# Kernel optimization log

Hardware: AMD Instinct MI355X
Metric: run time of the kernel (lower is better)

The kernel has to match this reference:

```python
import jax, jax.numpy as jnp
import numpy as np
import math

D_MODEL = 512
HEADS = 8
SHIFT = 1
B, T = 2, 1024


def _layernorm(x, w, b, eps=1e-5):
    mu = jnp.mean(x, -1, keepdims=True)
    var = jnp.mean((x - mu) ** 2, -1, keepdims=True)
    return (x - mu) / jnp.sqrt(var + eps) * w + b


def _l1_cdist(x, w, chunk):
    # x: [N, Din], w: [M, Din] -> [N, M]; chunk over M to bound the broadcast buffer
    N, Din = x.shape
    M = w.shape[0]
    wc = w.reshape(M // chunk, chunk, Din)
    f = lambda wb: jnp.abs(x[:, None, :] - wb[None, :, :]).sum(-1)  # [N, chunk]
    out = jax.lax.map(f, wc)  # [M//chunk, N, chunk]
    return jnp.moveaxis(out, 0, 1).reshape(N, M)


def _proxy_linear(x, w, gain, chunk):
    # ProxyDeltaLinearV68: out = (0.5 - dist_proxy_mean) * gain, dist uses detach trick
    Bx, Tx, Din = x.shape
    xa = jnp.tanh(x).reshape(-1, Din)
    wa = jnp.tanh(w)
    l1 = _l1_cdist(xa, wa, chunk)
    # squared L2 via GEMM (== cdist(p=2)**2), clamped at 0 like torch.cdist
    l2 = jnp.maximum((xa * xa).sum(-1)[:, None] + (wa * wa).sum(-1)[None, :] - 2.0 * (xa @ wa.T), 0.0)
    l1m = l1 / Din
    l2m = l2 / Din
    d = jax.lax.stop_gradient(l1m - l2m) + l2m
    return ((0.5 - d) * gain[None, :]).reshape(Bx, Tx, -1)


def _attention(x, wq_w, wq_g, wk_w, wk_g, wv_w, wv_g, wo_w, wo_b, gamma, rho):
    Bx, Tx, C = x.shape
    H, Dh = HEADS, C // HEADS

    def heads(t):
        return t.reshape(Bx, Tx, H, Dh).transpose(0, 2, 1, 3).reshape(Bx * H, Tx, Dh)

    q = heads(jnp.tanh(_proxy_linear(x, wq_w, wq_g, 32)))
    k = heads(jnp.tanh(_proxy_linear(x, wk_w, wk_g, 32)))
    v = heads(_proxy_linear(x, wv_w, wv_g, 32))
    # pairwise L1 distances, chunked over query positions
    TC = 64
    qr = jnp.moveaxis(q.reshape(Bx * H, Tx // TC, TC, Dh), 1, 0)  # [Tx//TC, BH, TC, Dh]
    f = lambda qb: jnp.abs(qb[:, :, None, :] - k[:, None, :, :]).sum(-1)  # [BH, TC, Tx]
    l1 = jnp.moveaxis(jax.lax.map(f, qr), 0, 1).reshape(Bx * H, Tx, Tx)
    l2 = jnp.maximum((q * q).sum(-1)[:, :, None] + (k * k).sum(-1)[:, None, :]
                     - 2.0 * jnp.einsum('btd,bsd->bts', q, k), 0.0)
    dist = jax.lax.stop_gradient((l1 - l2) / Dh) + l2 / Dh
    dist = dist.reshape(Bx, H, Tx, Tx) * math.sqrt(Dh)
    dsq = dist * dist
    gp = jax.nn.softplus(gamma)[None, :, None, None]
    rp = jax.nn.softplus(rho)[None, :, None, None]
    aw = (1.0 / (1.0 + gp * dsq + 1e-6)) ** rp  # student-t style kernel
    mask = jnp.tril(jnp.ones((Tx, Tx), dtype=bool))
    aw = jnp.where(mask[None, None], aw, 0.0)
    probs = aw / (aw.sum(-1, keepdims=True) + 1e-6)
    out = jnp.einsum('bhts,bhsd->bhtd', probs, v.reshape(Bx, H, Tx, Dh))
    out = out.transpose(0, 2, 1, 3).reshape(Bx, Tx, C)
    return out @ wo_w.T + wo_b


def setup_inputs() -> dict:
    key = jax.random.key(0)
    ks = jax.random.split(key, 10)
    D, Hd = D_MODEL, D_MODEL * 4
    f32 = jnp.float32
    return {
        'x': jax.random.normal(ks[0], (B, T, D), f32),
        'ln1_w': jnp.ones((D,), f32), 'ln1_b': jnp.zeros((D,), f32),
        'wq_w': jax.random.normal(ks[1], (D, D), f32) * 0.1, 'wq_g': jnp.full((D,), 2.0, f32),
        'wk_w': jax.random.normal(ks[2], (D, D), f32) * 0.1, 'wk_g': jnp.full((D,), 2.0, f32),
        'wv_w': jax.random.normal(ks[3], (D, D), f32) * 0.1, 'wv_g': jnp.full((D,), 2.0, f32),
        'wo_w': jax.random.normal(ks[4], (D, D), f32) * 0.02, 'wo_b': jnp.zeros((D,), f32),
        'gamma': jnp.ones((HEADS,), f32), 'rho': jnp.full((HEADS,), 2.0, f32),
        'ln2_w': jnp.ones((D,), f32), 'ln2_b': jnp.zeros((D,), f32),
        'gate_w': jax.random.normal(ks[5], (Hd, D), f32) * 0.1, 'gate_g': jnp.full((Hd,), 2.0, f32),
        'val_w': jax.random.normal(ks[6], (Hd, D), f32) * 0.1, 'val_g': jnp.full((Hd,), 2.0, f32),
        'out_w': jax.random.normal(ks[7], (D, Hd), f32) * 0.1, 'out_g': jnp.full((D,), 2.0, f32),
        'dir_w': jax.random.normal(ks[8], (D,), f32) * 0.1,
    }


def reference(x, ln1_w, ln1_b, wq_w, wq_g, wk_w, wk_g, wv_w, wv_g, wo_w, wo_b,
              gamma, rho, ln2_w, ln2_b, gate_w, gate_g, val_w, val_g, out_w, out_g, dir_w):
    a = _attention(_layernorm(x, ln1_w, ln1_b), wq_w, wq_g, wk_w, wk_g, wv_w, wv_g,
                   wo_w, wo_b, gamma, rho)
    x = x + a  # ATTN_SCALE = 1.0
    h = _layernorm(x, ln2_w, ln2_b)
    gate = jax.nn.silu(_proxy_linear(h, gate_w, gate_g, 32))
    val = _proxy_linear(h, val_w, val_g, 32)
    f = _proxy_linear(gate * val, out_w, out_g, 8)
    # Direction: causal shift of ln2 output, |x_shift - sigmoid(w)|
    xp = jnp.concatenate([jnp.zeros((x.shape[0], SHIFT, x.shape[2]), x.dtype), h[:, :-SHIFT]], axis=1)
    d = jnp.abs(xp - jax.nn.sigmoid(dir_w)[None, None, :])
    return x + f + 0.5 * d  # Delta_SCALE=1.0, DIR_SCALE=0.5, dropout identity (eval)
```

## Files before the change

### kernel.cpp

```cpp
#include <hip/hip_runtime.h>
#include <math.h>


#define NROWS  2048
#define DMODEL 512
#define TSEQ   1024
#define HIDDEN 2048

typedef _Float16 hf;
typedef hf h2 __attribute__((ext_vector_type(2)));
typedef hf h4 __attribute__((ext_vector_type(4)));
typedef hf h8 __attribute__((ext_vector_type(8)));
typedef float f32x4 __attribute__((ext_vector_type(4)));

#if defined(__has_builtin)
#if __has_builtin(__builtin_amdgcn_sad_u8)
#define HAVE_SAD 1
#endif
#if __has_builtin(__builtin_amdgcn_mfma_f32_16x16x32_f16)
#define HAVE_MFMA 1
#endif
#endif

__device__ __forceinline__ unsigned sad8(unsigned a, unsigned b, unsigned c) {
#ifdef HAVE_SAD
  return __builtin_amdgcn_sad_u8(a, b, c);
#else
  unsigned r;
  asm("v_sad_u8 %0, %1, %2, %3" : "=v"(r) : "v"(a), "v"(b), "v"(c));
  return r;
#endif
}

__device__ __forceinline__ float ftanh(float x) {
  const float t = __expf(-2.0f * fabsf(x));
  const float r = (1.0f - t) / (1.0f + t);
  return copysignf(r, x);
}

__device__ __forceinline__ float fpow_ge1(float x, float p) {
  float lg, r;
  asm("v_log_f32 %0, %1" : "=v"(lg) : "v"(x));
  const float e = lg * p;
  asm("v_exp_f32 %0, %1" : "=v"(r) : "v"(e));
  return r;
}

__device__ __forceinline__ unsigned q8(float x) {
  return (unsigned)(int)((x + 1.0f) * 127.5f + 0.5f);
}

struct CP { const float* g0; const float* g1; const float* g2; };

__global__ __launch_bounds__(256) void ln_kernel(
    const float* __restrict__ X, const float* __restrict__ w,
    const float* __restrict__ bb, float* __restrict__ outPlain,
    unsigned char* __restrict__ out8)
{
  const int n = blockIdx.x, tid = threadIdx.x;
  const float* row = X + (size_t)n * DMODEL;
  float2 v = *(const float2*)&row[tid * 2];
  float s1 = v.x + v.y;
  float s2 = v.x * v.x + v.y * v.y;
#pragma unroll
  for (int off = 1; off < 64; off <<= 1) {
    s1 += __shfl_xor(s1, off);
    s2 += __shfl_xor(s2, off);
  }
  __shared__ float red[8];
  if ((tid & 63) == 0) { red[(tid >> 6) * 2] = s1; red[(tid >> 6) * 2 + 1] = s2; }
  __syncthreads();
  s1 = red[0] + red[2] + red[4] + red[6];
  s2 = red[1] + red[3] + red[5] + red[7];
  const float mu   = s1 * (1.0f / DMODEL);
  const float var  = s2 * (1.0f / DMODEL) - mu * mu;
  const float rstd = rsqrtf(var + 1e-5f);
  const int d = tid * 2;
  const float y0 = (v.x - mu) * rstd * w[d]     + bb[d];
  const float y1 = (v.y - mu) * rstd * w[d + 1] + bb[d + 1];
  if (outPlain) *(float2*)&outPlain[(size_t)n * DMODEL + d] = make_float2(y0, y1);
  const unsigned a = q8(ftanh(y0)), b = q8(ftanh(y1));
  *(unsigned short*)&out8[(size_t)n * DMODEL + d] = (unsigned short)(a | (b << 8));
}

__global__ __launch_bounds__(256) void tanhcvt8m_kernel(
    const float* __restrict__ s0, const float* __restrict__ s1,
    const float* __restrict__ s2, unsigned char* __restrict__ out, int K)
{
  const int z = blockIdx.y;
  const float* sb = (z == 0) ? s0 : (z == 1) ? s1 : s2;
  const int rows = (int)gridDim.x * 2;
  const int row = blockIdx.x * 2 + (threadIdx.x >> 7);
  const int t = threadIdx.x & 127;
  const float* src = sb + (size_t)row * K;
  unsigned char* dst = out + ((size_t)z * rows + row) * K;
  for (int k = t * 4; k < K; k += 512) {
    float4 v = *(const float4*)&src[k];
    unsigned pk = q8(ftanh(v.x)) | (q8(ftanh(v.y)) << 8) |
                  (q8(ftanh(v.z)) << 16) | (q8(ftanh(v.w)) << 24);
    *(unsigned*)&dst[k] = pk;
  }
}

template <int NCD, int EPI>
__global__ __launch_bounds__(256, 8) void cdistn_kernel(
    const unsigned char* __restrict__ X8, const unsigned char* __restrict__ W8,
    CP cp,
    unsigned char* __restrict__ o8a, unsigned char* __restrict__ o8b,
    hf* __restrict__ vt16, unsigned char* __restrict__ gvt8,
    unsigned short* __restrict__ pf,
    int M, int K, int Kc, float invK127)
{
  const int m0 = blockIdx.x * 32, n0 = blockIdx.y * 64;
  const int zc = (EPI == 1) ? blockIdx.z : 0;
  const int kb = (EPI == 3) ? blockIdx.z * Kc : 0;
  __shared__ unsigned xs8[2][8][68];
  __shared__ unsigned ws8[2][8][NCD * 36];
  const int tid = threadIdx.x, tx = tid & 15, ty = tid >> 4;
  unsigned acc[NCD][4][2] = {};

  const int rs = tid >> 2, pxs = (tid & 3) * 2;
  const int half = tid & 127;
  const int wc = (NCD == 2) ? (tid >> 7) : 0;
  const int wcol = half >> 2, pws = (half & 3) * 2;

  const unsigned char* xp = X8 + (size_t)(n0 + rs) * K + kb + (tid & 3) * 8;
  const unsigned char* wq = W8 + (size_t)(zc + wc) * M * K +
                            (size_t)(m0 + wcol) * K + kb + (half & 3) * 8;

  uint2 xv = *(const uint2*)xp;
  uint2 wv = *(const uint2*)wq;

  int p = 0;
#pragma unroll 1
  for (int k0 = 0; k0 < Kc; k0 += 32) {
    xs8[p][pxs + 0][rs] = xv.x;
    xs8[p][pxs + 1][rs] = xv.y;
    ws8[p][pws + 0][wc * 36 + wcol] = wv.x;
    ws8[p][pws + 1][wc * 36 + wcol] = wv.y;
    const int kn = (k0 + 32 < Kc) ? k0 + 32 : 0;
    xv = *(const uint2*)(xp + kn);
    wv = *(const uint2*)(wq + kn);
    __syncthreads();

#pragma unroll
    for (int kk = 0; kk < 8; kk++) {
      uint4 a4 = *(const uint4*)&xs8[p][kk][ty * 4];
      const unsigned a[4] = {a4.x, a4.y, a4.z, a4.w};
#pragma unroll
      for (int c = 0; c < NCD; c++) {
        uint2 b2 = *(const uint2*)&ws8[p][kk][c * 36 + tx * 2];
        const unsigned bb[2] = {b2.x, b2.y};
#pragma unroll
        for (int i = 0; i < 4; i++)
#pragma unroll
          for (int j = 0; j < 2; j++)
            acc[c][i][j] = sad8(a[i], bb[j], acc[c][i][j]);
      }
    }
    p ^= 1;
  }

  if constexpr (EPI == 1) {
    if (zc < 2) {
      unsigned char* o8 = zc ? o8b : o8a;
      const float* gn = zc ? cp.g1 : cp.g0;
#pragma unroll
      for (int i = 0; i < 4; i++) {
        const int n = n0 + ty * 4 + i;
        unsigned pk = 0;
#pragma unroll
        for (int j = 0; j < 2; j++) {
          const int m = m0 + tx * 2 + j;
          const float val = (0.5f - (float)acc[0][i][j] * invK127) * gn[m];
          pk |= q8(ftanh(val)) << (8 * j);
        }
        *(unsigned short*)&o8[(size_t)n * M + m0 + tx * 2] = (unsigned short)pk;
      }
    } else {
#pragma unroll
      for (int i = 0; i < 4; i++) {
        const int n = n0 + ty * 4 + i;
        const int b = n >> 10, t = n & 1023;
#pragma unroll
        for (int j = 0; j < 2; j++) {
          const int m = m0 + tx * 2 + j;
          const float vv = (0.5f - (float)acc[0][i][j] * invK127) * cp.g2[m];
          vt16[((size_t)(b * 8 + (m >> 6)) * 64 + (m & 63)) * 1024 + t] = (hf)vv;
        }
      }
    }
  } else if constexpr (EPI == 2) {
#pragma unroll
    for (int i = 0; i < 4; i++) {
      const int n = n0 + ty * 4 + i;
      unsigned pk = 0;
#pragma unroll
      for (int j = 0; j < 2; j++) {
        const int m = m0 + tx * 2 + j;
        float g = (0.5f - (float)acc[0][i][j] * invK127) * cp.g0[m];
        g = g / (1.0f + __expf(-g));
        const float vv = (0.5f - (float)acc[1][i][j] * invK127) * cp.g1[m];
        pk |= q8(ftanh(g * vv)) << (8 * j);
      }
      *(unsigned short*)&gvt8[(size_t)n * M + m0 + tx * 2] = (unsigned short)pk;
    }
  } else {
    unsigned short* pz = pf + (size_t)blockIdx.z * ((size_t)NROWS * M);
#pragma unroll
    for (int i = 0; i < 4; i++) {
      const int n = n0 + ty * 4 + i;
      const unsigned p0 = (acc[0][i][0] + 1) >> 1;
      const unsigned p1 = (acc[0][i][1] + 1) >> 1;
      *(unsigned*)&pz[(size_t)n * M + m0 + tx * 2] = p0 | (p1 << 16);
    }
  }
}

__global__ __launch_bounds__(256) void attn_part_kernel(
    const unsigned char* __restrict__ Qb, const unsigned char* __restrict__ Kb,
    const hf* __restrict__ Vt,
    const float* __restrict__ gamma, const float* __restrict__ rho,
    float* __restrict__ accO, float* __restrict__ accR)
{
  const int bh = blockIdx.y, b = bh >> 3, h = bh & 7;
  int rem = 143 - (int)blockIdx.x;
  int tt = 0;
  for (;;) {
    const int nc = ((tt >> 1) + 2) >> 1;
    if (rem < nc) break;
    rem -= nc; ++tt;
  }
  const int ntile = (tt >> 1) + 1;
  const int sb = rem * 2;
  const int se = (sb + 2 < ntile) ? sb + 2 : ntile;
  const int t0 = tt * 32;

  const float gp = log1pf(expf(gamma[h]));
  const float nrp = -log1pf(expf(rho[h]));
  const size_t base8 = ((size_t)b * TSEQ) * DMODEL + h * 64;

  __shared__ unsigned qs8[16][36];
  __shared__ unsigned ks8[16][68];
  __shared__ hf awt[32][72];
  __shared__ hf vsm[64][72];

  const int tid = threadIdx.x, tx = tid & 15, ty = tid >> 4;
  const int tx4 = tx * 4, ty2 = ty * 2;
  const int lane = tid & 63, wv = tid >> 6;
  const float SCALE_D = 1.0f / (127.5f * 8.0f);

  {
    const int r = tid >> 3, p = (tid & 7) * 2;
    uint2 a = *(const uint2*)&Qb[base8 + (size_t)(t0 + r) * DMODEL + (tid & 7) * 8];
    qs8[p + 0][r] = a.x;
    qs8[p + 1][r] = a.y;
  }

  float rsum[2] = {};
  f32x4 cacc[2] = {};

  const int vd = tid >> 2, vs16 = (tid & 3) * 16;
  const int arow = lane & 15;
  const int koff = (lane >> 4) * 8;

  for (int st = sb; st < se; ++st) {
    const int s0 = st * 64;
    __syncthreads();
    {
      const int r = tid >> 2, p = (tid & 3) * 4;
      uint4 a = *(const uint4*)&Kb[base8 + (size_t)(s0 + r) * DMODEL + (tid & 3) * 16];
      ks8[p + 0][r] = a.x;
      ks8[p + 1][r] = a.y;
      ks8[p + 2][r] = a.z;
      ks8[p + 3][r] = a.w;
      const hf* vsrc = &Vt[((size_t)bh * 64 + vd) * 1024 + s0 + vs16];
      *(h8*)&vsm[vd][vs16 + 0] = *(const h8*)vsrc;
      *(h8*)&vsm[vd][vs16 + 8] = *(const h8*)(vsrc + 8);
    }
    __syncthreads();

    unsigned sacc[2][4] = {};
#pragma unroll
    for (int kk = 0; kk < 16; kk++) {
      uint2 qa = *(const uint2*)&qs8[kk][ty2];
      uint4 kb4 = *(const uint4*)&ks8[kk][tx4];
      const unsigned kk4[4] = {kb4.x, kb4.y, kb4.z, kb4.w};
#pragma unroll
      for (int j = 0; j < 4; j++) {
        sacc[0][j] = sad8(qa.x, kk4[j], sacc[0][j]);
        sacc[1][j] = sad8(qa.y, kk4[j], sacc[1][j]);
      }
    }

#pragma unroll
    for (int i = 0; i < 2; i++) {
      const int tg = t0 + ty2 + i;
      h4 pk;
#pragma unroll
      for (int j = 0; j < 4; j++) {
        const int sg = s0 + tx4 + j;
        const float dist = (float)sacc[i][j] * SCALE_D;
        const float bsx = fmaf(gp, dist * dist, 1.0f + 1e-6f);
        float aw = fpow_ge1(bsx, nrp);
        aw = (sg <= tg) ? aw : 0.0f;
        pk[j] = (hf)aw;
        rsum[i] += aw;
      }
      *(h4*)&awt[ty2 + i][tx4] = pk;
    }
    __syncthreads();

#ifdef HAVE_MFMA
#pragma unroll
    for (int ks = 0; ks < 2; ks++) {
      h8 bfrag = *(const h8*)&vsm[wv * 16 + arow][ks * 32 + koff];
      h8 afr0  = *(const h8*)&awt[arow]          [ks * 32 + koff];
      h8 afr1  = *(const h8*)&awt[16 + arow]     [ks * 32 + koff];
      cacc[0] = __builtin_amdgcn_mfma_f32_16x16x32_f16(afr0, bfrag, cacc[0], 0, 0, 0);
      cacc[1] = __builtin_amdgcn_mfma_f32_16x16x32_f16(afr1, bfrag, cacc[1], 0, 0, 0);
    }
#else
    {
      const int crow = (lane >> 4) * 4;
      const int d = wv * 16 + (lane & 15);
#pragma unroll
      for (int mt = 0; mt < 2; mt++)
#pragma unroll
        for (int r = 0; r < 4; r++) {
          const int t = mt * 16 + crow + r;
          float s = cacc[mt][r];
          for (int si = 0; si < 64; si++)
            s += (float)awt[t][si] * (float)vsm[d][si];
          cacc[mt][r] = s;
        }
    }
#endif
  }

#pragma unroll
  for (int off = 1; off < 16; off <<= 1) {
    rsum[0] += __shfl_xor(rsum[0], off);
    rsum[1] += __shfl_xor(rsum[1], off);
  }
  float* aO = accO + ((size_t)bh * TSEQ + t0) * 64;
  {
    const int crow = (lane >> 4) * 4;
    const int ccol = wv * 16 + (lane & 15);
#pragma unroll
    for (int mt = 0; mt < 2; mt++)
#pragma unroll
      for (int r = 0; r < 4; r++)
        atomicAdd(&aO[(size_t)(mt * 16 + crow + r) * 64 + ccol], cacc[mt][r]);
  }
#pragma unroll
  for (int i = 0; i < 2; i++)
    if (tx == 0) atomicAdd(&accR[bh * TSEQ + t0 + ty2 + i], rsum[i]);
}

__global__ __launch_bounds__(256) void gemm_res_kernel(
    const float* __restrict__ Xn, const float* __restrict__ accR,
    const float* __restrict__ W,
    const float* __restrict__ bias, const float* __restrict__ Res,
    float* __restrict__ Out)
{
  const int m0 = blockIdx.x * 64, n0 = blockIdx.y * 64;
  __shared__ float xs[16][68];
  __shared__ float wsm[16][68];
  const int tid = threadIdx.x, tx = tid & 15, ty = tid >> 4;
  const int lr = tid >> 2, lc4 = (tid & 3) * 4;
  float acc[4][4] = {};
  const int n = n0 + lr;
  const float* wp = &W[(size_t)(m0 + lr) * DMODEL + lc4];
  for (int k0 = 0; k0 < DMODEL; k0 += 16) {
    const int c = k0 + lc4;
    const size_t arow = ((size_t)((n >> 10) * 8 + (c >> 6))) * TSEQ + (n & 1023);
    float4 xv = *(const float4*)&Xn[arow * 64 + (c & 63)];
    const float inv = 1.0f / (accR[arow] + 1e-6f);
    xv.x *= inv; xv.y *= inv; xv.z *= inv; xv.w *= inv;
    float4 wv = *(const float4*)(wp + k0);
    __syncthreads();
    xs [lc4 + 0][lr] = xv.x; xs [lc4 + 1][lr] = xv.y; xs [lc4 + 2][lr] = xv.z; xs [lc4 + 3][lr] = xv.w;
    wsm[lc4 + 0][lr] = wv.x; wsm[lc4 + 1][lr] = wv.y; wsm[lc4 + 2][lr] = wv.z; wsm[lc4 + 3][lr] = wv.w;
    __syncthreads();
#pragma unroll
    for (int kk = 0; kk < 16; kk++) {
      float4 av = *(const float4*)&xs[kk][ty * 4];
      float4 bv = *(const float4*)&wsm[kk][tx * 4];
      const float aa[4] = {av.x, av.y, av.z, av.w};
      const float bs[4] = {bv.x, bv.y, bv.z, bv.w};
#pragma unroll
      for (int i = 0; i < 4; i++)
#pragma unroll
        for (int j = 0; j < 4; j++) acc[i][j] = fmaf(aa[i], bs[j], acc[i][j]);
    }
  }
#pragma unroll
  for (int i = 0; i < 4; i++) {
    const int nn = n0 + ty * 4 + i;
    float o[4];
#pragma unroll
    for (int j = 0; j < 4; j++) {
      const int m = m0 + tx * 4 + j;
      o[j] = acc[i][j] + bias[m] + Res[(size_t)nn * DMODEL + m];
    }
    *(float4*)&Out[(size_t)nn * DMODEL + m0 + tx * 4] = make_float4(o[0], o[1], o[2], o[3]);
  }
}

__global__ void final_kernel(const float* __restrict__ x2,
                             const unsigned short* __restrict__ pf,
                             const float* __restrict__ outg,
                             const float* __restrict__ h,
                             const float* __restrict__ dirw,
                             float* __restrict__ out)
{
  const int i4 = blockIdx.x * 256 + threadIdx.x;
  const int n = i4 >> 7;
  const int t = n & (TSEQ - 1);
  const int d4 = (i4 & 127) * 4;
  float4 xv = *(const float4*)&x2[(size_t)i4 * 4];
  const size_t off = (size_t)i4 * 4;
  unsigned s[4] = {};
#pragma unroll
  for (int z = 0; z < 4; z++) {
    uint2 a = *(const uint2*)&pf[(size_t)z * ((size_t)NROWS * DMODEL) + off];
    s[0] += (a.x & 0xffffu);
    s[1] += (a.x >> 16);
    s[2] += (a.y & 0xffffu);
    s[3] += (a.y >> 16);
  }
  float4 hv = make_float4(0.f, 0.f, 0.f, 0.f);
  if (t != 0) hv = *(const float4*)&h[(size_t)(i4 - 128) * 4];
  const float xx[4] = {xv.x, xv.y, xv.z, xv.w};
  const float hh[4] = {hv.x, hv.y, hv.z, hv.w};
  const float invf = 2.0f / (127.5f * 2048.0f);
  float o[4];
#pragma unroll
  for (int j = 0; j < 4; j++) {
    const float f = (0.5f - (float)s[j] * invf) * outg[d4 + j];
    const float sg = 1.0f / (1.0f + __expf(-dirw[d4 + j]));
    o[j] = xx[j] + f + 0.5f * fabsf(hh[j] - sg);
  }
  *(float4*)&out[(size_t)i4 * 4] = make_float4(o[0], o[1], o[2], o[3]);
}

extern "C" void kernel_launch(void* const* d_in, const int* in_sizes, int n_in,
                              void* d_out, int out_size, void* d_ws, size_t ws_size,
                              hipStream_t stream)
{
  (void)in_sizes; (void)n_in; (void)out_size;
  const float* x      = (const float*)d_in[0];
  const float* ln1_w  = (const float*)d_in[1];
  const float* ln1_b  = (const float*)d_in[2];
  const float* wq_w   = (const float*)d_in[3];
  const float* wq_g   = (const float*)d_in[4];
  const float* wk_w   = (const float*)d_in[5];
  const float* wk_g   = (const float*)d_in[6];
  const float* wv_w   = (const float*)d_in[7];
  const float* wv_g   = (const float*)d_in[8];
  const float* wo_w   = (const float*)d_in[9];
  const float* wo_b   = (const float*)d_in[10];
  const float* gamma  = (const float*)d_in[11];
  const float* rho    = (const float*)d_in[12];
  const float* ln2_w  = (const float*)d_in[13];
  const float* ln2_b  = (const float*)d_in[14];
  const float* gate_w = (const float*)d_in[15];
  const float* gate_g = (const float*)d_in[16];
  const float* val_w  = (const float*)d_in[17];
  const float* val_g  = (const float*)d_in[18];
  const float* out_w  = (const float*)d_in[19];
  const float* out_g  = (const float*)d_in[20];
  const float* dir_w  = (const float*)d_in[21];
  float* out = (float*)d_out;

  if (ws_size < ((size_t)32 << 20)) return;
  unsigned char* wsb = (unsigned char*)d_ws;

  unsigned char* w8   = wsb;
  unsigned char* x8   = wsb + ((size_t)2 << 20);
  unsigned char* q8b  = wsb + ((size_t)3 << 20);
  unsigned char* k8b  = wsb + ((size_t)4 << 20);
  hf*            vt16 = (hf*)(wsb + ((size_t)5 << 20));
  unsigned char* gvt8 = wsb + ((size_t)7 << 20);
  float*         accO = (float*)(wsb + ((size_t)11 << 20));
  float*         accR = (float*)(wsb + ((size_t)15 << 20));
  unsigned short* pf  = (unsigned short*)(wsb + ((size_t)16 << 20));
  float*         x2   = (float*)(wsb + ((size_t)24 << 20));
  float*         hbuf = (float*)(wsb + ((size_t)28 << 20));

  ln_kernel<<<NROWS, 256, 0, stream>>>(x, ln1_w, ln1_b, nullptr, x8);

  tanhcvt8m_kernel<<<dim3(256, 3), 256, 0, stream>>>(wq_w, wk_w, wv_w, w8, 512);

  {
    CP cp; cp.g0 = wq_g; cp.g1 = wk_g; cp.g2 = wv_g;
    cdistn_kernel<1, 1><<<dim3(16, 32, 3), 256, 0, stream>>>(
        x8, w8, cp, q8b, k8b, vt16, nullptr, nullptr,
        512, 512, 512, 1.0f / (127.5f * 512.0f));
  }

  hipMemsetAsync(accO, 0, (size_t)(16 * TSEQ * 64 + 16 * TSEQ) * sizeof(float), stream);
  attn_part_kernel<<<dim3(144, 16), 256, 0, stream>>>(q8b, k8b, vt16,
                                                      gamma, rho, accO, accR);

  gemm_res_kernel<<<dim3(8, 32), 256, 0, stream>>>(accO, accR, wo_w, wo_b, x, x2);

  ln_kernel<<<NROWS, 256, 0, stream>>>(x2, ln2_w, ln2_b, hbuf, x8);

  tanhcvt8m_kernel<<<dim3(1024, 2), 256, 0, stream>>>(gate_w, val_w, val_w, w8, 512);

  {
    CP cp; cp.g0 = gate_g; cp.g1 = val_g; cp.g2 = nullptr;
    cdistn_kernel<2, 2><<<dim3(64, 32, 1), 256, 0, stream>>>(
        x8, w8, cp, nullptr, nullptr, nullptr, gvt8, nullptr,
        2048, 512, 512, 1.0f / (127.5f * 512.0f));
  }

  tanhcvt8m_kernel<<<dim3(256, 1), 256, 0, stream>>>(out_w, out_w, out_w, w8, 2048);

  {
    CP cp; cp.g0 = out_g; cp.g1 = nullptr; cp.g2 = nullptr;
    cdistn_kernel<1, 3><<<dim3(16, 32, 4), 256, 0, stream>>>(
        gvt8, w8, cp, nullptr, nullptr, nullptr, nullptr, pf,
        512, 2048, 512, 0.0f);
  }

  final_kernel<<<1024, 256, 0, stream>>>(x2, pf, out_g, hbuf, dir_w, out);
}
```

Measured before the change: 165.2 us.

## Make cdist tiles wave-private to drop block barriers; fold accumulator zeroing into LayerNorm

The SAD-based cdist kernel now gives each wavefront its own 16-row shared-memory slice and loads its own copy of the full 32-column weight tile, so the per-iteration __syncthreads and double buffering are removed. The cost is that each wave reloads the whole weight tile, which multiplies weight global loads and LDS writes by four. Separately, the hipMemsetAsync that cleared the attention accumulators is dropped, and the first LayerNorm kernel zeroes that buffer as a side task. This saves one launch.

```diff
diff --git a/kernel.cpp b/kernel.cpp
--- a/kernel.cpp
+++ b/kernel.cpp
@@ -55,9 +55,11 @@
 __global__ __launch_bounds__(256) void ln_kernel(
     const float* __restrict__ X, const float* __restrict__ w,
     const float* __restrict__ bb, float* __restrict__ outPlain,
-    unsigned char* __restrict__ out8)
+    unsigned char* __restrict__ out8, float4* __restrict__ zf)
 {
   const int n = blockIdx.x, tid = threadIdx.x;
+  if (zf && tid < 130)
+    zf[(size_t)n * 130 + tid] = make_float4(0.f, 0.f, 0.f, 0.f);
   const float* row = X + (size_t)n * DMODEL;
   float2 v = *(const float2*)&row[tid * 2];
   float s1 = v.x + v.y;
@@ -103,7 +105,7 @@
 }
 
 template <int NCD, int EPI>
-__global__ __launch_bounds__(256, 8) void cdistn_kernel(
+__global__ __launch_bounds__(256, 8) void cdistp_kernel(
     const unsigned char* __restrict__ X8, const unsigned char* __restrict__ W8,
     CP cp,
     unsigned char* __restrict__ o8a, unsigned char* __restrict__ o8b,
@@ -114,42 +116,59 @@
   const int m0 = blockIdx.x * 32, n0 = blockIdx.y * 64;
   const int zc = (EPI == 1) ? blockIdx.z : 0;
   const int kb = (EPI == 3) ? blockIdx.z * Kc : 0;
-  __shared__ unsigned xs8[2][8][68];
-  __shared__ unsigned ws8[2][8][NCD * 36];
+  constexpr int REPS = NCD * 2;
+  constexpr int WW = NCD * 36 + 2;
+  __shared__ unsigned xs[4][8][20];
+  __shared__ unsigned ws[4][8][WW];
   const int tid = threadIdx.x, tx = tid & 15, ty = tid >> 4;
+  const int lane = tid & 63, wv = tid >> 6;
+  const int tyw = ty & 3;
   unsigned acc[NCD][4][2] = {};
 
-  const int rs = tid >> 2, pxs = (tid & 3) * 2;
-  const int half = tid & 127;
-  const int wc = (NCD == 2) ? (tid >> 7) : 0;
-  const int wcol = half >> 2, pws = (half & 3) * 2;
-
-  const unsigned char* xp = X8 + (size_t)(n0 + rs) * K + kb + (tid & 3) * 8;
-  const unsigned char* wq = W8 + (size_t)(zc + wc) * M * K +
-                            (size_t)(m0 + wcol) * K + kb + (half & 3) * 8;
+  const int xr = lane >> 2, pxs = (lane & 3) * 2;
+  const unsigned char* xp = X8 + (size_t)(n0 + wv * 16 + xr) * K + kb + (lane & 3) * 8;
+
+  const unsigned char* wqb = W8 + (size_t)zc * M * K + (size_t)m0 * K + kb;
+  unsigned woff[REPS];
+  int wpw[REPS], wcb[REPS];
+#pragma unroll
+  for (int r = 0; r < REPS; r++) {
+    const int idx = lane + 64 * r;
+    const int c = idx >> 7;
+    const int rem = idx & 127;
+    const int col = rem >> 2, pw = (rem & 3) * 2;
+    woff[r] = (unsigned)(c * M * K + col * K + pw * 4);
+    wpw[r] = pw;
+    wcb[r] = c * 36 + col;
+  }
 
   uint2 xv = *(const uint2*)xp;
-  uint2 wv = *(const uint2*)wq;
-
-  int p = 0;
+  uint2 wvr[REPS];
+#pragma unroll
+  for (int r = 0; r < REPS; r++) wvr[r] = *(const uint2*)(wqb + woff[r]);
+
 #pragma unroll 1
   for (int k0 = 0; k0 < Kc; k0 += 32) {
-    xs8[p][pxs + 0][rs] = xv.x;
-    xs8[p][pxs + 1][rs] = xv.y;
-    ws8[p][pws + 0][wc * 36 + wcol] = wv.x;
-    ws8[p][pws + 1][wc * 36 + wcol] = wv.y;
+    xs[wv][pxs + 0][xr] = xv.x;
+    xs[wv][pxs + 1][xr] = xv.y;
+#pragma unroll
+    for (int r = 0; r < REPS; r++) {
+      ws[wv][wpw[r] + 0][wcb[r]] = wvr[r].x;
+      ws[wv][wpw[r] + 1][wcb[r]] = wvr[r].y;
+    }
     const int kn = (k0 + 32 < Kc) ? k0 + 32 : 0;
     xv = *(const uint2*)(xp + kn);
-    wv = *(const uint2*)(wq + kn);
-    __syncthreads();
+#pragma unroll
+    for (int r = 0; r < REPS; r++)
+      wvr[r] = *(const uint2*)(wqb + woff[r] + kn);
 
 #pragma unroll
     for (int kk = 0; kk < 8; kk++) {
-      uint4 a4 = *(const uint4*)&xs8[p][kk][ty * 4];
+      uint4 a4 = *(const uint4*)&xs[wv][kk][tyw * 4];
       const unsigned a[4] = {a4.x, a4.y, a4.z, a4.w};
 #pragma unroll
       for (int c = 0; c < NCD; c++) {
-        uint2 b2 = *(const uint2*)&ws8[p][kk][c * 36 + tx * 2];
+        uint2 b2 = *(const uint2*)&ws[wv][kk][c * 36 + tx * 2];
         const unsigned bb[2] = {b2.x, b2.y};
 #pragma unroll
         for (int i = 0; i < 4; i++)
@@ -158,7 +177,6 @@
             acc[c][i][j] = sad8(a[i], bb[j], acc[c][i][j]);
       }
     }
-    p ^= 1;
   }
 
   if constexpr (EPI == 1) {
@@ -489,30 +507,30 @@
   float*         x2   = (float*)(wsb + ((size_t)24 << 20));
   float*         hbuf = (float*)(wsb + ((size_t)28 << 20));
 
-  ln_kernel<<<NROWS, 256, 0, stream>>>(x, ln1_w, ln1_b, nullptr, x8);
+  ln_kernel<<<NROWS, 256, 0, stream>>>(x, ln1_w, ln1_b, nullptr, x8,
+                                       (float4*)accO);
 
   tanhcvt8m_kernel<<<dim3(256, 3), 256, 0, stream>>>(wq_w, wk_w, wv_w, w8, 512);
 
   {
     CP cp; cp.g0 = wq_g; cp.g1 = wk_g; cp.g2 = wv_g;
-    cdistn_kernel<1, 1><<<dim3(16, 32, 3), 256, 0, stream>>>(
+    cdistp_kernel<1, 1><<<dim3(16, 32, 3), 256, 0, stream>>>(
         x8, w8, cp, q8b, k8b, vt16, nullptr, nullptr,
         512, 512, 512, 1.0f / (127.5f * 512.0f));
   }
 
-  hipMemsetAsync(accO, 0, (size_t)(16 * TSEQ * 64 + 16 * TSEQ) * sizeof(float), stream);
   attn_part_kernel<<<dim3(144, 16), 256, 0, stream>>>(q8b, k8b, vt16,
                                                       gamma, rho, accO, accR);
 
   gemm_res_kernel<<<dim3(8, 32), 256, 0, stream>>>(accO, accR, wo_w, wo_b, x, x2);
 
-  ln_kernel<<<NROWS, 256, 0, stream>>>(x2, ln2_w, ln2_b, hbuf, x8);
+  ln_kernel<<<NROWS, 256, 0, stream>>>(x2, ln2_w, ln2_b, hbuf, x8, nullptr);
 
   tanhcvt8m_kernel<<<dim3(1024, 2), 256, 0, stream>>>(gate_w, val_w, val_w, w8, 512);
 
   {
     CP cp; cp.g0 = gate_g; cp.g1 = val_g; cp.g2 = nullptr;
-    cdistn_kernel<2, 2><<<dim3(64, 32, 1), 256, 0, stream>>>(
+    cdistp_kernel<2, 2><<<dim3(64, 32, 1), 256, 0, stream>>>(
         x8, w8, cp, nullptr, nullptr, nullptr, gvt8, nullptr,
         2048, 512, 512, 1.0f / (127.5f * 512.0f));
   }
@@ -521,7 +539,7 @@
 
   {
     CP cp; cp.g0 = out_g; cp.g1 = nullptr; cp.g2 = nullptr;
-    cdistn_kernel<1, 3><<<dim3(16, 32, 4), 256, 0, stream>>>(
+    cdistp_kernel<1, 3><<<dim3(16, 32, 4), 256, 0, stream>>>(
         gvt8, w8, cp, nullptr, nullptr, nullptr, nullptr, pf,
         512, 2048, 512, 0.0f);
   }
```

New measurement: 167.6 us. Within noise of the previous version (+1.4%).
